# Performance work log

Measured on AMD Instinct MI355X. Metric: run time of the kernel, lower is better.

The kernel has to match this reference:

```python
import jax, jax.numpy as jnp
import numpy as np

B, A, STATE_LEN, H, REL_LEN, E = 32, 64, 256, 128, 64, 16

def _mlp2(x, w1, b1, w2, b2):
    # DI-engine MLP, 2 layers, ReLU after every layer (incl. output)
    return jax.nn.relu(jax.nn.relu(x @ w1 + b1) @ w2 + b2)

def setup_inputs() -> dict:
    key = jax.random.key(0)
    ks = jax.random.split(key, 16)
    def w(k, fi, fo):
        return (jax.random.normal(k, (fi, fo), jnp.float32) / np.float32(np.sqrt(fi)))
    z = lambda n: jnp.zeros((n,), jnp.float32)
    return {
        "states": jax.random.normal(ks[0], (B, A, STATE_LEN), jnp.float32),
        "relations": jax.random.normal(ks[1], (B, A, A, REL_LEN), jnp.float32),
        "alive_mask": (jax.random.uniform(ks[2], (B, A)) > 0.3).astype(jnp.float32),
        "se_w1": w(ks[3], STATE_LEN, H), "se_b1": z(H),
        "se_w2": w(ks[4], H, H), "se_b2": z(H),
        "re_w1": w(ks[5], H + REL_LEN, H), "re_b1": z(H),
        "re_w2": w(ks[6], H, 2 * H), "re_b2": z(2 * H),
        "ra_w": w(ks[7], 3 * H, H), "ra_b": z(H),
        "ae_w1": w(ks[8], 4 * H, H), "ae_b1": z(H),
        "ae_w2": w(ks[9], H, 2 * H), "ae_b2": z(2 * H),
        "action_embed": jax.random.normal(ks[10], (E, H), jnp.float32) * np.float32(np.sqrt(2.0 / H)),
        "action_mask": jnp.ones((B, A, E + A), jnp.int32),
        "action": jax.random.randint(ks[11], (B,), 0, E + A),
        "agent_id": 0,
    }

def reference(states, relations, alive_mask,
              se_w1, se_b1, se_w2, se_b2,
              re_w1, re_b1, re_w2, re_b2,
              ra_w, ra_b,
              ae_w1, ae_b1, ae_w2, ae_b2,
              action_embed, action_mask, action, agent_id):
    del action_mask  # read by the torch module but never used
    b, a = states.shape[0], states.shape[1]
    h, e = se_w2.shape[1], action_embed.shape[0]
    # encode per-agent state: [B,A,H]
    s = _mlp2(states, se_w1, se_b1, se_w2, se_b2)
    # relation encoder: concat target-agent state onto each relation edge
    rel_in = jnp.concatenate(
        [relations, jnp.broadcast_to(s[:, None], (b, a, a, h))], axis=-1)
    r = _mlp2(rel_in, re_w1, re_b1, re_w2, re_b2)               # [B,A,A,2H]
    # relation aggregator: masked mean / masked max over source agents
    r_avr, r_max = jnp.split(r, 2, axis=-1)
    m = alive_mask[:, None, :, None]                             # [B,1,A,1]
    r_avr = (r_avr * m).mean(axis=-2)                            # [B,A,H]
    r_max = (r_max * m).max(axis=-2)                             # [B,A,H]
    s = jax.nn.relu(jnp.concatenate([s, r_avr, r_max], axis=-1) @ ra_w + ra_b)
    # pairwise action embeddings: [B,A,A,2H]
    ae_in = jnp.concatenate(
        [r,
         jnp.broadcast_to(s[:, None], (b, a, a, h)),
         jnp.broadcast_to(s[:, :, None], (b, a, a, h))], axis=-1)
    ae = _mlp2(ae_in, ae_w1, ae_b1, ae_w2, ae_b2)
    active, passive = jnp.split(ae, 2, axis=-1)                  # [B,A,A,H] each
    # acting agent `agent_id`: candidates = [embed_num self actions | A targeted actions]
    active_i = active[:, agent_id]                               # [B,A,H]
    active_full = jnp.concatenate(
        [jnp.broadcast_to(action_embed[None], (b, e, h)), active_i], axis=1)  # [B,E+A,H]
    sel = jnp.take_along_axis(active_full, action[:, None, None], axis=1)     # [B,1,H]
    state = s.at[:, agent_id].add(sel[:, 0])
    # passive side: target j receives passive embed iff action == E + j, else zero
    passive_i = passive[:, agent_id]                             # [B,A,H]
    hit = (action[:, None] == (e + jnp.arange(a))[None, :])      # [B,A]
    passive_sel = jnp.where(hit[:, :, None], passive_i, jnp.zeros((), states.dtype))
    state = state + passive_sel
    return state, sel[:, :, None], passive_sel
```

## Files before the change

kernel.cpp:

```cpp
#include <hip/hip_runtime.h>

#define NB 32
#define NA 64
#define SLEN 256
#define NH 128
#define RLEN 64
#define NE 16

typedef _Float16 f16;
typedef _Float16 f16x8 __attribute__((ext_vector_type(8)));
typedef _Float16 f16x4 __attribute__((ext_vector_type(4)));
typedef float f32x4 __attribute__((ext_vector_type(4)));

__device__ inline f16x8 cvt8(float4 a, float4 b) {
  f16x8 r;
  r[0] = (f16)a.x; r[1] = (f16)a.y; r[2] = (f16)a.z; r[3] = (f16)a.w;
  r[4] = (f16)b.x; r[5] = (f16)b.y; r[6] = (f16)b.z; r[7] = (f16)b.w;
  return r;
}

__device__ inline void gload_lds16(const float* g, float* l) {
  __builtin_amdgcn_global_load_lds((const __attribute__((address_space(1))) void*)g,
                                   (__attribute__((address_space(3))) void*)l, 16, 0, 0);
}

__global__ __launch_bounds__(256) void k0_pack(const float* __restrict__ re_w1,
                                               const float* __restrict__ re_w2,
                                               const float* __restrict__ se_w1,
                                               const float* __restrict__ se_w2,
                                               const float* __restrict__ ra_w,
                                               const float* __restrict__ ae_w1,
                                               const float* __restrict__ ae_w2,
                                               f16* __restrict__ pk) {
  int idx = blockIdx.x * 256 + threadIdx.x;
  const float* src;
  int ro, N, ld, base;
  if (idx < 8192)        { src = re_w1; ro = 0;   N = 128; ld = 128; base = 0; }
  else if (idx < 40960)  { src = re_w2; ro = 0;   N = 256; ld = 256; base = 8192; }
  else if (idx < 73728)  { src = se_w1; ro = 0;   N = 128; ld = 128; base = 40960; }
  else if (idx < 90112)  { src = se_w2; ro = 0;   N = 128; ld = 128; base = 73728; }
  else if (idx < 106496) { src = re_w1; ro = 64;  N = 128; ld = 128; base = 90112; }
  else if (idx < 155648) { src = ra_w;  ro = 0;   N = 128; ld = 128; base = 106496; }
  else if (idx < 172032) { src = ae_w1; ro = 256; N = 128; ld = 128; base = 155648; }
  else if (idx < 188416) { src = ae_w1; ro = 384; N = 128; ld = 128; base = 172032; }
  else if (idx < 221184) { src = ae_w1; ro = 0;   N = 128; ld = 128; base = 188416; }
  else if (idx < 253952) { src = ae_w2; ro = 0;   N = 256; ld = 256; base = 221184; }
  else return;
  int li = idx - base;
  int t = li & 7, l = (li >> 3) & 63, rem = li >> 9;
  int NT = N >> 4;
  int nt = rem % NT, kt = rem / NT;
  int k = kt * 32 + (l >> 4) * 8 + t;
  int n = nt * 16 + (l & 15);
  pk[idx] = (f16)src[(size_t)(ro + k) * ld + n];
}

__global__ __launch_bounds__(256) void k1m(const float* __restrict__ states,
                                           const float* __restrict__ se_b1,
                                           const float* __restrict__ se_b2,
                                           const float* __restrict__ re_b1,
                                           const f16* __restrict__ pse1,
                                           const f16* __restrict__ pse2,
                                           const f16* __restrict__ pre1b,
                                           float* __restrict__ s_out,
                                           float* __restrict__ sp_pk) {
  __shared__ f16 t1[16 * 128];
  __shared__ f16 t2[16 * 128];
  const int row0 = blockIdx.x * 16;
  const int tid = threadIdx.x;
  const int w = tid >> 6, l = tid & 63, lr = l & 15, lh = l >> 4;

  f32x4 acc[2];
  acc[0] = (f32x4){0.f, 0.f, 0.f, 0.f};
  acc[1] = (f32x4){0.f, 0.f, 0.f, 0.f};

#pragma unroll
  for (int kt = 0; kt < 8; ++kt) {
    const float* p = states + (size_t)(row0 + lr) * SLEN + kt * 32 + lh * 8;
    f16x8 aF = cvt8(*(const float4*)p, *(const float4*)(p + 4));
#pragma unroll
    for (int n = 0; n < 2; ++n) {
      f16x8 bF = *(const f16x8*)(pse1 + ((size_t)(kt * 8 + w * 2 + n) * 64 + l) * 8);
      acc[n] = __builtin_amdgcn_mfma_f32_16x16x32_f16(aF, bF, acc[n], 0, 0, 0);
    }
  }
#pragma unroll
  for (int n = 0; n < 2; ++n) {
    int h = w * 32 + n * 16 + lr;
    float bias = se_b1[h];
#pragma unroll
    for (int reg = 0; reg < 4; ++reg) {
      int j = lh * 4 + reg;
      float v = fmaxf(acc[n][reg] + bias, 0.f);
      unsigned off = (unsigned)((j * NH + h) * 2) ^ ((unsigned)(j & 7) << 4);
      *(f16*)((char*)t1 + off) = (f16)v;
    }
  }
  __syncthreads();

  acc[0] = (f32x4){0.f, 0.f, 0.f, 0.f};
  acc[1] = (f32x4){0.f, 0.f, 0.f, 0.f};
#pragma unroll
  for (int kt = 0; kt < 4; ++kt) {
    unsigned off = (unsigned)((lr * NH + kt * 32 + lh * 8) * 2) ^ ((unsigned)(lr & 7) << 4);
    f16x8 aF = *(const f16x8*)((char*)t1 + off);
#pragma unroll
    for (int n = 0; n < 2; ++n) {
      f16x8 bF = *(const f16x8*)(pse2 + ((size_t)(kt * 8 + w * 2 + n) * 64 + l) * 8);
      acc[n] = __builtin_amdgcn_mfma_f32_16x16x32_f16(aF, bF, acc[n], 0, 0, 0);
    }
  }
#pragma unroll
  for (int n = 0; n < 2; ++n) {
    int h = w * 32 + n * 16 + lr;
    float bias = se_b2[h];
#pragma unroll
    for (int reg = 0; reg < 4; ++reg) {
      int j = lh * 4 + reg;
      float v = fmaxf(acc[n][reg] + bias, 0.f);
      s_out[(size_t)(row0 + j) * NH + h] = v;
      unsigned off = (unsigned)((j * NH + h) * 2) ^ ((unsigned)(j & 7) << 4);
      *(f16*)((char*)t2 + off) = (f16)v;
    }
  }
  __syncthreads();

  acc[0] = (f32x4){0.f, 0.f, 0.f, 0.f};
  acc[1] = (f32x4){0.f, 0.f, 0.f, 0.f};
#pragma unroll
  for (int kt = 0; kt < 4; ++kt) {
    unsigned off = (unsigned)((lr * NH + kt * 32 + lh * 8) * 2) ^ ((unsigned)(lr & 7) << 4);
    f16x8 aF = *(const f16x8*)((char*)t2 + off);
#pragma unroll
    for (int n = 0; n < 2; ++n) {
      f16x8 bF = *(const f16x8*)(pre1b + ((size_t)(kt * 8 + w * 2 + n) * 64 + l) * 8);
      acc[n] = __builtin_amdgcn_mfma_f32_16x16x32_f16(aF, bF, acc[n], 0, 0, 0);
    }
  }
  const int bb = row0 >> 6;
  const int mtile = (row0 & 63) >> 4;
#pragma unroll
  for (int n = 0; n < 2; ++n) {
    int h = w * 32 + n * 16 + lr;
    float bias = re_b1[h];
    float4 outv;
#pragma unroll
    for (int reg = 0; reg < 4; ++reg) outv[reg] = acc[n][reg] + bias;
    *(float4*)(sp_pk + ((size_t)((bb * 4 + mtile) * 8 + w * 2 + n) * 64 + l) * 4) = outv;
  }
}

__global__ __launch_bounds__(256) void k3_rel(const float* __restrict__ relations,
                                              const float* __restrict__ alive_mask,
                                              const float* __restrict__ sp_pk,
                                              const float* __restrict__ re_b2,
                                              const f16* __restrict__ pw1,
                                              const f16* __restrict__ pw2,
                                              const int* __restrict__ agent_id,
                                              float* __restrict__ r_red,
                                              f16* __restrict__ r_agent) {
  __shared__ float relb[2][64 * 64];
  __shared__ f16 tl[64 * 128];
  __shared__ float alive[NA];
  const int bid = blockIdx.x;
  const int b = bid >> 4;
  const int i0 = (bid & 15) * 4;
  const int tid = threadIdx.x;
  const int w = tid >> 6, l = tid & 63, lr = l & 15, lh = l >> 4;

  auto stage = [&](int buf, int i) {
    const float* g = relations + (size_t)(b * NA + i) * NA * RLEN;
#pragma unroll
    for (int c4 = 0; c4 < 4; ++c4) {
      int c = w * 4 + c4;
      int srcf = c * 256 + ((l ^ ((4 * c + (l >> 4)) & 7)) * 4);
      gload_lds16(g + srcf, &relb[buf][c * 256]);
    }
  };

  stage(0, i0);
  if (tid < 64) alive[tid] = alive_mask[b * NA + tid];
  float bz[4];
#pragma unroll
  for (int n = 0; n < 4; ++n) bz[n] = re_b2[w * 64 + n * 16 + lr];
  f16x8 b1f[2][2];
#pragma unroll
  for (int kt = 0; kt < 2; ++kt)
#pragma unroll
    for (int n = 0; n < 2; ++n)
      b1f[kt][n] = *(const f16x8*)(pw1 + ((size_t)(kt * 8 + w * 2 + n) * 64 + l) * 8);
  float4 sp4[4][2];
  {
    const float* spp = sp_pk + (size_t)b * 8192;
#pragma unroll
    for (int mt = 0; mt < 4; ++mt)
#pragma unroll
      for (int n = 0; n < 2; ++n)
        sp4[mt][n] = *(const float4*)(spp + (size_t)((mt * 8 + w * 2 + n) * 64 + l) * 4);
  }
  const int aid = agent_id[0];
  const bool domax = (w >= 2);
  __syncthreads();

  for (int t = 0; t < 4; ++t) {
    const int cur = t & 1;
    f32x4 acc1[4][2];
#pragma unroll
    for (int mt = 0; mt < 4; ++mt)
#pragma unroll
      for (int n = 0; n < 2; ++n) acc1[mt][n] = (f32x4){0.f, 0.f, 0.f, 0.f};
#pragma unroll
    for (int mt = 0; mt < 4; ++mt) {
      int R = mt * 16 + lr;
      unsigned sw = ((unsigned)(R & 7)) << 4;
      f16x8 aK[2];
#pragma unroll
      for (int kt = 0; kt < 2; ++kt) {
        unsigned base = (unsigned)((R * 64 + kt * 32 + lh * 8) * 4);
        float4 v0 = *(const float4*)((char*)relb[cur] + (base ^ sw));
        float4 v1 = *(const float4*)((char*)relb[cur] + ((base + 16) ^ sw));
        aK[kt] = cvt8(v0, v1);
      }
#pragma unroll
      for (int kt = 0; kt < 2; ++kt)
#pragma unroll
        for (int n = 0; n < 2; ++n)
          acc1[mt][n] = __builtin_amdgcn_mfma_f32_16x16x32_f16(aK[kt], b1f[kt][n],
                                                               acc1[mt][n], 0, 0, 0);
    }
#pragma unroll
    for (int mt = 0; mt < 4; ++mt)
#pragma unroll
      for (int n = 0; n < 2; ++n) {
        int h = w * 32 + n * 16 + lr;
#pragma unroll
        for (int reg = 0; reg < 4; ++reg) {
          int j = mt * 16 + lh * 4 + reg;
          float v = fmaxf(acc1[mt][n][reg] + sp4[mt][n][reg], 0.f);
          unsigned off = (unsigned)((j * NH + h) * 2) ^ ((unsigned)(j & 7) << 4);
          *(f16*)((char*)tl + off) = (f16)v;
        }
      }
    __syncthreads();

    if (t < 3) stage(cur ^ 1, i0 + t + 1);

    f32x4 acc2[4][4];
#pragma unroll
    for (int mt = 0; mt < 4; ++mt)
#pragma unroll
      for (int n = 0; n < 4; ++n) acc2[mt][n] = (f32x4){0.f, 0.f, 0.f, 0.f};
#pragma unroll
    for (int kt2 = 0; kt2 < 4; ++kt2) {
      f16x8 a2[4];
#pragma unroll
      for (int mt = 0; mt < 4; ++mt) {
        int row = mt * 16 + lr;
        unsigned off = (unsigned)((row * 256 + kt2 * 64 + lh * 16)) ^ ((unsigned)(row & 7) << 4);
        a2[mt] = *(const f16x8*)((char*)tl + off);
      }
      f16x8 b2f[4];
#pragma unroll
      for (int n = 0; n < 4; ++n)
        b2f[n] = *(const f16x8*)(pw2 + ((size_t)(kt2 * 16 + w * 4 + n) * 64 + l) * 8);
#pragma unroll
      for (int mt = 0; mt < 4; ++mt)
#pragma unroll
        for (int n = 0; n < 4; ++n)
          acc2[mt][n] = __builtin_amdgcn_mfma_f32_16x16x32_f16(a2[mt], b2f[n], acc2[mt][n], 0, 0, 0);
    }

    const int i = i0 + t;
    const bool isagent = (i == aid);
    float red[4];
#pragma unroll
    for (int n = 0; n < 4; ++n) red[n] = 0.f;
#pragma unroll
    for (int n = 0; n < 4; ++n) {
      int col = w * 64 + n * 16 + lr;
      float bias = bz[n];
#pragma unroll
      for (int mt = 0; mt < 4; ++mt)
#pragma unroll
        for (int reg = 0; reg < 4; ++reg) {
          int j = mt * 16 + lh * 4 + reg;
          float rv = fmaxf(acc2[mt][n][reg] + bias, 0.f);
          float rm = rv * alive[j];
          red[n] = domax ? fmaxf(red[n], rm) : (red[n] + rm);
          if (isagent) r_agent[((size_t)b * NA + j) * 256 + col] = (f16)rv;
        }
    }
#pragma unroll
    for (int n = 0; n < 4; ++n) {
      float v = red[n];
      float v1 = __shfl_xor(v, 16, 64);
      v = domax ? fmaxf(v, v1) : v + v1;
      float v2 = __shfl_xor(v, 32, 64);
      v = domax ? fmaxf(v, v2) : v + v2;
      if (lh == 0) r_red[(size_t)(b * NA + i) * 256 + w * 64 + n * 16 + lr] = v;
    }
    __syncthreads();
  }
}

__global__ __launch_bounds__(256) void k4m(const float* __restrict__ s,
                                           const float* __restrict__ r_red,
                                           const float* __restrict__ ra_b,
                                           const f16* __restrict__ pra,
                                           float* __restrict__ s_new) {
  __shared__ f16 x3[16 * 384];
  const int row0 = blockIdx.x * 16;
  const int tid = threadIdx.x;
  const int w = tid >> 6, l = tid & 63, lr = l & 15, lh = l >> 4;

#pragma unroll
  for (int it = 0; it < 6; ++it) {
    int e = it * 1024 + tid * 4;
    int row = e / 384;
    int c = e - row * 384;
    float4 v;
    if (c < 128) {
      v = *(const float4*)(s + (size_t)(row0 + row) * NH + c);
    } else {
      v = *(const float4*)(r_red + (size_t)(row0 + row) * 256 + (c - 128));
      if (c < 256) { v.x *= (1.f / 64.f); v.y *= (1.f / 64.f); v.z *= (1.f / 64.f); v.w *= (1.f / 64.f); }
    }
    f16x4 hv;
    hv[0] = (f16)v.x; hv[1] = (f16)v.y; hv[2] = (f16)v.z; hv[3] = (f16)v.w;
    unsigned off = (unsigned)((row * 384 + c) * 2) ^ ((unsigned)(row & 7) << 4);
    *(f16x4*)((char*)x3 + off) = hv;
  }
  __syncthreads();

  f32x4 acc[2];
  acc[0] = (f32x4){0.f, 0.f, 0.f, 0.f};
  acc[1] = (f32x4){0.f, 0.f, 0.f, 0.f};
#pragma unroll
  for (int kt = 0; kt < 12; ++kt) {
    unsigned off = (unsigned)((lr * 384 + kt * 32 + lh * 8) * 2) ^ ((unsigned)(lr & 7) << 4);
    f16x8 aF = *(const f16x8*)((char*)x3 + off);
#pragma unroll
    for (int n = 0; n < 2; ++n) {
      f16x8 bF = *(const f16x8*)(pra + ((size_t)(kt * 8 + w * 2 + n) * 64 + l) * 8);
      acc[n] = __builtin_amdgcn_mfma_f32_16x16x32_f16(aF, bF, acc[n], 0, 0, 0);
    }
  }
#pragma unroll
  for (int n = 0; n < 2; ++n) {
    int h = w * 32 + n * 16 + lr;
    float bias = ra_b[h];
#pragma unroll
    for (int reg = 0; reg < 4; ++reg) {
      int j = lh * 4 + reg;
      s_new[(size_t)(row0 + j) * NH + h] = fmaxf(acc[n][reg] + bias, 0.f);
    }
  }
}

__global__ __launch_bounds__(256) void k5m(const f16* __restrict__ r_agent,
                                           const float* __restrict__ s_new,
                                           const float* __restrict__ ae_b1,
                                           const float* __restrict__ ae_b2,
                                           const float* __restrict__ action_embed,
                                           const int* __restrict__ action,
                                           const int* __restrict__ agent_id,
                                           const f16* __restrict__ pae1a,
                                           const f16* __restrict__ pae1b,
                                           const f16* __restrict__ pae1c,
                                           const f16* __restrict__ pae2,
                                           float* __restrict__ sel_ws,
                                           float* __restrict__ pas_ws,
                                           float* __restrict__ out_sel) {
  __shared__ f16 xa[16 * 512];
  __shared__ f16 t1[16 * 128];
  __shared__ int actL[16];
  const int b0 = blockIdx.x * 16;
  const int tid = threadIdx.x;
  const int w = tid >> 6, l = tid & 63, lr = l & 15, lh = l >> 4;
  const int aid = agent_id[0];

  {
    int row = tid & 15, g = tid >> 4;
    int bb = b0 + row;
    int act = action[bb];
    if (g == 0) actL[row] = act;
    int jj = act >= NE ? act - NE : 0;
    int k0 = g * 32;
    f16x8 vv[4];
    if (g < 8) {
      const f16* src = r_agent + ((size_t)bb * NA + jj) * 256 + k0;
#pragma unroll
      for (int c = 0; c < 4; ++c) vv[c] = *(const f16x8*)(src + c * 8);
    } else {
      const float* src = (g < 12) ? (s_new + ((size_t)bb * NA + jj) * NH + (g - 8) * 32)
                                  : (s_new + ((size_t)bb * NA + aid) * NH + (g - 12) * 32);
#pragma unroll
      for (int c = 0; c < 4; ++c)
        vv[c] = cvt8(*(const float4*)(src + c * 8), *(const float4*)(src + c * 8 + 4));
    }
#pragma unroll
    for (int c = 0; c < 4; ++c) {
      unsigned off = (unsigned)((row * 512 + k0 + c * 8) * 2) ^ ((unsigned)(row & 7) << 4);
      *(f16x8*)((char*)xa + off) = vv[c];
    }
  }
  __syncthreads();

  f32x4 acc[2];
  acc[0] = (f32x4){0.f, 0.f, 0.f, 0.f};
  acc[1] = (f32x4){0.f, 0.f, 0.f, 0.f};
#pragma unroll
  for (int kt = 0; kt < 16; ++kt) {
    unsigned off = (unsigned)((lr * 512 + kt * 32 + lh * 8) * 2) ^ ((unsigned)(lr & 7) << 4);
    f16x8 aF = *(const f16x8*)((char*)xa + off);
    const f16* pseg = (kt < 8) ? pae1a : (kt < 12) ? pae1b : pae1c;
    int ktl = (kt < 8) ? kt : (kt < 12) ? kt - 8 : kt - 12;
#pragma unroll
    for (int n = 0; n < 2; ++n) {
      f16x8 bF = *(const f16x8*)(pseg + ((size_t)(ktl * 8 + w * 2 + n) * 64 + l) * 8);
      acc[n] = __builtin_amdgcn_mfma_f32_16x16x32_f16(aF, bF, acc[n], 0, 0, 0);
    }
  }
#pragma unroll
  for (int n = 0; n < 2; ++n) {
    int h = w * 32 + n * 16 + lr;
    float bias = ae_b1[h];
#pragma unroll
    for (int reg = 0; reg < 4; ++reg) {
      int j = lh * 4 + reg;
      float v = fmaxf(acc[n][reg] + bias, 0.f);
      unsigned off = (unsigned)((j * NH + h) * 2) ^ ((unsigned)(j & 7) << 4);
      *(f16*)((char*)t1 + off) = (f16)v;
    }
  }
  __syncthreads();

  f32x4 acc2[4];
#pragma unroll
  for (int n = 0; n < 4; ++n) acc2[n] = (f32x4){0.f, 0.f, 0.f, 0.f};
#pragma unroll
  for (int kt = 0; kt < 4; ++kt) {
    unsigned off = (unsigned)((lr * NH + kt * 32 + lh * 8) * 2) ^ ((unsigned)(lr & 7) << 4);
    f16x8 aF = *(const f16x8*)((char*)t1 + off);
#pragma unroll
    for (int n = 0; n < 4; ++n) {
      f16x8 bF = *(const f16x8*)(pae2 + ((size_t)(kt * 16 + w * 4 + n) * 64 + l) * 8);
      acc2[n] = __builtin_amdgcn_mfma_f32_16x16x32_f16(aF, bF, acc2[n], 0, 0, 0);
    }
  }
#pragma unroll
  for (int n = 0; n < 4; ++n) {
    int col = w * 64 + n * 16 + lr;
    float bias = ae_b2[col];
#pragma unroll
    for (int reg = 0; reg < 4; ++reg) {
      int row = lh * 4 + reg;
      int bb = b0 + row;
      int act = actL[row];
      float v = fmaxf(acc2[n][reg] + bias, 0.f);
      if (col < NH) {
        float sv = (act < NE) ? action_embed[act * NH + col] : v;
        sel_ws[bb * NH + col] = sv;
        out_sel[bb * NH + col] = sv;
      } else {
        pas_ws[bb * NH + col - NH] = (act < NE) ? 0.f : v;
      }
    }
  }
}

__global__ __launch_bounds__(256) void k5g(const int* __restrict__ action,
                                           const int* __restrict__ agent_id,
                                           const float* __restrict__ sel_ws,
                                           const float* __restrict__ pas_ws,
                                           const float* __restrict__ s_new,
                                           float* __restrict__ out_state,
                                           float* __restrict__ out_passive) {
  int q = blockIdx.x * 256 + threadIdx.x;
  int idx = q * 4;
  int h = idx & 127;
  int row = idx >> 7;
  int b = row >> 6, i = row & 63;
  int act = action[b];
  int aid = agent_id[0];
  float4 st = *(const float4*)(s_new + idx);
  float4 ps = {0.f, 0.f, 0.f, 0.f};
  if (act >= NE && i == act - NE) {
    ps = *(const float4*)(pas_ws + b * NH + h);
    st.x += ps.x; st.y += ps.y; st.z += ps.z; st.w += ps.w;
  }
  if (i == aid) {
    const float4 sl = *(const float4*)(sel_ws + b * NH + h);
    st.x += sl.x; st.y += sl.y; st.z += sl.z; st.w += sl.w;
  }
  *(float4*)(out_state + idx) = st;
  *(float4*)(out_passive + idx) = ps;
}

extern "C" void kernel_launch(void* const* d_in, const int* in_sizes, int n_in,
                              void* d_out, int out_size, void* d_ws, size_t ws_size,
                              hipStream_t stream) {
  (void)in_sizes; (void)n_in; (void)out_size; (void)ws_size;
  const float* states       = (const float*)d_in[0];
  const float* relations    = (const float*)d_in[1];
  const float* alive_mask   = (const float*)d_in[2];
  const float* se_w1        = (const float*)d_in[3];
  const float* se_b1        = (const float*)d_in[4];
  const float* se_w2        = (const float*)d_in[5];
  const float* se_b2        = (const float*)d_in[6];
  const float* re_w1        = (const float*)d_in[7];
  const float* re_b1        = (const float*)d_in[8];
  const float* re_w2        = (const float*)d_in[9];
  const float* re_b2        = (const float*)d_in[10];
  const float* ra_w         = (const float*)d_in[11];
  const float* ra_b         = (const float*)d_in[12];
  const float* ae_w1        = (const float*)d_in[13];
  const float* ae_b1        = (const float*)d_in[14];
  const float* ae_w2        = (const float*)d_in[15];
  const float* ae_b2        = (const float*)d_in[16];
  const float* action_embed = (const float*)d_in[17];
  const int*   action       = (const int*)d_in[19];
  const int*   agent_id     = (const int*)d_in[20];
  float* out = (float*)d_out;

  float* wsf     = (float*)d_ws;
  float* s       = wsf;
  float* sp_pk   = wsf + 262144;
  float* r_red   = wsf + 524288;
  float* s_new   = wsf + 1048576;
  float* sel_ws  = wsf + 1310720;
  float* pas_ws  = wsf + 1314816;
  f16*   wsh     = (f16*)(wsf + 1318912);
  f16*   r_agent = wsh;
  f16*   pk      = wsh + 524288;
  f16*   pw_re1a = pk;
  f16*   pw_re2  = pk + 8192;
  f16*   pw_se1  = pk + 40960;
  f16*   pw_se2  = pk + 73728;
  f16*   pw_re1b = pk + 90112;
  f16*   pw_ra   = pk + 106496;
  f16*   pw_ae1b = pk + 155648;
  f16*   pw_ae1c = pk + 172032;
  f16*   pw_ae1a = pk + 188416;
  f16*   pw_ae2  = pk + 221184;

  k0_pack<<<992, 256, 0, stream>>>(re_w1, re_w2, se_w1, se_w2, ra_w, ae_w1, ae_w2, pk);
  k1m<<<128, 256, 0, stream>>>(states, se_b1, se_b2, re_b1, pw_se1, pw_se2, pw_re1b,
                               s, sp_pk);
  k3_rel<<<512, 256, 0, stream>>>(relations, alive_mask, sp_pk, re_b2, pw_re1a, pw_re2,
                                  agent_id, r_red, r_agent);
  k4m<<<128, 256, 0, stream>>>(s, r_red, ra_b, pw_ra, s_new);
  k5m<<<2, 256, 0, stream>>>(r_agent, s_new, ae_b1, ae_b2, action_embed, action,
                             agent_id, pw_ae1a, pw_ae1b, pw_ae1c, pw_ae2,
                             sel_ws, pas_ws, out + 262144);
  k5g<<<256, 256, 0, stream>>>(action, agent_id, sel_ws, pas_ws, s_new,
                               out, out + 266240);
}
```

Baseline: 168.1 us.

## Fuse weight packing into state encoder and merge final gather into action kernel

The standalone pack kernel is merged into the state-encoder kernel: extra blocks pack the weights used by later kernels, while the encoder reads its own weights directly from fp32 global memory using strided gathers. The final scatter kernel is folded into the action-embedding kernel, with extra blocks copying the untouched rows and the two compute blocks writing the special rows from shared memory. This removes two kernel launches and the workspace round-trip for sel/passive, at the cost of uncoalesced strided weight loads in the encoder.

```diff
diff --git a/kernel.cpp b/kernel.cpp
--- a/kernel.cpp
+++ b/kernel.cpp
@@ -24,48 +24,50 @@
                                    (__attribute__((address_space(3))) void*)l, 16, 0, 0);
 }
 
-__global__ __launch_bounds__(256) void k0_pack(const float* __restrict__ re_w1,
-                                               const float* __restrict__ re_w2,
-                                               const float* __restrict__ se_w1,
-                                               const float* __restrict__ se_w2,
-                                               const float* __restrict__ ra_w,
-                                               const float* __restrict__ ae_w1,
-                                               const float* __restrict__ ae_w2,
-                                               f16* __restrict__ pk) {
-  int idx = blockIdx.x * 256 + threadIdx.x;
-  const float* src;
-  int ro, N, ld, base;
-  if (idx < 8192)        { src = re_w1; ro = 0;   N = 128; ld = 128; base = 0; }
-  else if (idx < 40960)  { src = re_w2; ro = 0;   N = 256; ld = 256; base = 8192; }
-  else if (idx < 73728)  { src = se_w1; ro = 0;   N = 128; ld = 128; base = 40960; }
-  else if (idx < 90112)  { src = se_w2; ro = 0;   N = 128; ld = 128; base = 73728; }
-  else if (idx < 106496) { src = re_w1; ro = 64;  N = 128; ld = 128; base = 90112; }
-  else if (idx < 155648) { src = ra_w;  ro = 0;   N = 128; ld = 128; base = 106496; }
-  else if (idx < 172032) { src = ae_w1; ro = 256; N = 128; ld = 128; base = 155648; }
-  else if (idx < 188416) { src = ae_w1; ro = 384; N = 128; ld = 128; base = 172032; }
-  else if (idx < 221184) { src = ae_w1; ro = 0;   N = 128; ld = 128; base = 188416; }
-  else if (idx < 253952) { src = ae_w2; ro = 0;   N = 256; ld = 256; base = 221184; }
-  else return;
-  int li = idx - base;
-  int t = li & 7, l = (li >> 3) & 63, rem = li >> 9;
-  int NT = N >> 4;
-  int nt = rem % NT, kt = rem / NT;
-  int k = kt * 32 + (l >> 4) * 8 + t;
-  int n = nt * 16 + (l & 15);
-  pk[idx] = (f16)src[(size_t)(ro + k) * ld + n];
-}
-
-__global__ __launch_bounds__(256) void k1m(const float* __restrict__ states,
-                                           const float* __restrict__ se_b1,
-                                           const float* __restrict__ se_b2,
-                                           const float* __restrict__ re_b1,
-                                           const f16* __restrict__ pse1,
-                                           const f16* __restrict__ pse2,
-                                           const f16* __restrict__ pre1b,
-                                           float* __restrict__ s_out,
-                                           float* __restrict__ sp_pk) {
+__device__ inline f16x8 gatherW(const float* __restrict__ W, int ld, int row0, int col) {
+  f16x8 r;
+#pragma unroll
+  for (int t = 0; t < 8; ++t) r[t] = (f16)W[(size_t)(row0 + t) * ld + col];
+  return r;
+}
+
+__global__ __launch_bounds__(256) void ka(const float* __restrict__ states,
+                                          const float* __restrict__ se_w1,
+                                          const float* __restrict__ se_b1,
+                                          const float* __restrict__ se_w2,
+                                          const float* __restrict__ se_b2,
+                                          const float* __restrict__ re_w1,
+                                          const float* __restrict__ re_b1,
+                                          const float* __restrict__ re_w2,
+                                          const float* __restrict__ ra_w,
+                                          const float* __restrict__ ae_w1,
+                                          const float* __restrict__ ae_w2,
+                                          float* __restrict__ s_out,
+                                          float* __restrict__ sp_pk,
+                                          f16* __restrict__ pk) {
   __shared__ f16 t1[16 * 128];
   __shared__ f16 t2[16 * 128];
+  if (blockIdx.x >= 128) {
+    int t0 = (blockIdx.x - 128) * 256 + threadIdx.x;
+    for (int idx = t0; idx < 188416; idx += 64 * 256) {
+      const float* src; int ro, N, ld, base, dst;
+      if (idx < 8192)        { src = re_w1; ro = 0;   N = 128; ld = 128; base = 0;      dst = 0; }
+      else if (idx < 40960)  { src = re_w2; ro = 0;   N = 256; ld = 256; base = 8192;   dst = 8192; }
+      else if (idx < 90112)  { src = ra_w;  ro = 0;   N = 128; ld = 128; base = 40960;  dst = 106496; }
+      else if (idx < 106496) { src = ae_w1; ro = 256; N = 128; ld = 128; base = 90112;  dst = 155648; }
+      else if (idx < 122880) { src = ae_w1; ro = 384; N = 128; ld = 128; base = 106496; dst = 172032; }
+      else if (idx < 155648) { src = ae_w1; ro = 0;   N = 128; ld = 128; base = 122880; dst = 188416; }
+      else                   { src = ae_w2; ro = 0;   N = 256; ld = 256; base = 155648; dst = 221184; }
+      int li = idx - base;
+      int t = li & 7, l = (li >> 3) & 63, rem = li >> 9;
+      int NT = N >> 4;
+      int nt = rem % NT, kt = rem / NT;
+      int k = kt * 32 + (l >> 4) * 8 + t;
+      int n = nt * 16 + (l & 15);
+      pk[dst + li] = (f16)src[(size_t)(ro + k) * ld + n];
+    }
+    return;
+  }
   const int row0 = blockIdx.x * 16;
   const int tid = threadIdx.x;
   const int w = tid >> 6, l = tid & 63, lr = l & 15, lh = l >> 4;
@@ -80,7 +82,7 @@
     f16x8 aF = cvt8(*(const float4*)p, *(const float4*)(p + 4));
 #pragma unroll
     for (int n = 0; n < 2; ++n) {
-      f16x8 bF = *(const f16x8*)(pse1 + ((size_t)(kt * 8 + w * 2 + n) * 64 + l) * 8);
+      f16x8 bF = gatherW(se_w1, 128, kt * 32 + lh * 8, (w * 2 + n) * 16 + lr);
       acc[n] = __builtin_amdgcn_mfma_f32_16x16x32_f16(aF, bF, acc[n], 0, 0, 0);
     }
   }
@@ -106,7 +108,7 @@
     f16x8 aF = *(const f16x8*)((char*)t1 + off);
 #pragma unroll
     for (int n = 0; n < 2; ++n) {
-      f16x8 bF = *(const f16x8*)(pse2 + ((size_t)(kt * 8 + w * 2 + n) * 64 + l) * 8);
+      f16x8 bF = gatherW(se_w2, 128, kt * 32 + lh * 8, (w * 2 + n) * 16 + lr);
       acc[n] = __builtin_amdgcn_mfma_f32_16x16x32_f16(aF, bF, acc[n], 0, 0, 0);
     }
   }
@@ -133,7 +135,7 @@
     f16x8 aF = *(const f16x8*)((char*)t2 + off);
 #pragma unroll
     for (int n = 0; n < 2; ++n) {
-      f16x8 bF = *(const f16x8*)(pre1b + ((size_t)(kt * 8 + w * 2 + n) * 64 + l) * 8);
+      f16x8 bF = gatherW(re_w1, 128, 64 + kt * 32 + lh * 8, (w * 2 + n) * 16 + lr);
       acc[n] = __builtin_amdgcn_mfma_f32_16x16x32_f16(aF, bF, acc[n], 0, 0, 0);
     }
   }
@@ -357,27 +359,46 @@
   }
 }
 
-__global__ __launch_bounds__(256) void k5m(const f16* __restrict__ r_agent,
-                                           const float* __restrict__ s_new,
-                                           const float* __restrict__ ae_b1,
-                                           const float* __restrict__ ae_b2,
-                                           const float* __restrict__ action_embed,
-                                           const int* __restrict__ action,
-                                           const int* __restrict__ agent_id,
-                                           const f16* __restrict__ pae1a,
-                                           const f16* __restrict__ pae1b,
-                                           const f16* __restrict__ pae1c,
-                                           const f16* __restrict__ pae2,
-                                           float* __restrict__ sel_ws,
-                                           float* __restrict__ pas_ws,
-                                           float* __restrict__ out_sel) {
+__global__ __launch_bounds__(256) void k5mg(const f16* __restrict__ r_agent,
+                                            const float* __restrict__ s_new,
+                                            const float* __restrict__ ae_b1,
+                                            const float* __restrict__ ae_b2,
+                                            const float* __restrict__ action_embed,
+                                            const int* __restrict__ action,
+                                            const int* __restrict__ agent_id,
+                                            const f16* __restrict__ pae1a,
+                                            const f16* __restrict__ pae1b,
+                                            const f16* __restrict__ pae1c,
+                                            const f16* __restrict__ pae2,
+                                            float* __restrict__ out_state,
+                                            float* __restrict__ out_sel,
+                                            float* __restrict__ out_passive) {
   __shared__ f16 xa[16 * 512];
   __shared__ f16 t1[16 * 128];
+  __shared__ float selL[16][128];
+  __shared__ float pasL[16][128];
   __shared__ int actL[16];
+  const int aid = agent_id[0];
+  const int tid = threadIdx.x;
+
+  if (blockIdx.x >= 2) {
+    int q = (blockIdx.x - 2) * 256 + tid;
+    int idx = q * 4;
+    int h = idx & 127;
+    int row = idx >> 7;
+    int b = row >> 6, i = row & 63;
+    int act = action[b];
+    bool special = (i == aid) || (act >= NE && i == act - NE);
+    if (!special) {
+      *(float4*)(out_state + idx) = *(const float4*)(s_new + idx);
+      *(float4*)(out_passive + idx) = (float4){0.f, 0.f, 0.f, 0.f};
+    }
+    (void)h;
+    return;
+  }
+
   const int b0 = blockIdx.x * 16;
-  const int tid = threadIdx.x;
   const int w = tid >> 6, l = tid & 63, lr = l & 15, lh = l >> 4;
-  const int aid = agent_id[0];
 
   {
     int row = tid & 15, g = tid >> 4;
@@ -455,46 +476,33 @@
 #pragma unroll
     for (int reg = 0; reg < 4; ++reg) {
       int row = lh * 4 + reg;
-      int bb = b0 + row;
       int act = actL[row];
       float v = fmaxf(acc2[n][reg] + bias, 0.f);
       if (col < NH) {
-        float sv = (act < NE) ? action_embed[act * NH + col] : v;
-        sel_ws[bb * NH + col] = sv;
-        out_sel[bb * NH + col] = sv;
+        selL[row][col] = (act < NE) ? action_embed[act * NH + col] : v;
       } else {
-        pas_ws[bb * NH + col - NH] = (act < NE) ? 0.f : v;
+        pasL[row][col - NH] = (act < NE) ? 0.f : v;
       }
     }
   }
-}
-
-__global__ __launch_bounds__(256) void k5g(const int* __restrict__ action,
-                                           const int* __restrict__ agent_id,
-                                           const float* __restrict__ sel_ws,
-                                           const float* __restrict__ pas_ws,
-                                           const float* __restrict__ s_new,
-                                           float* __restrict__ out_state,
-                                           float* __restrict__ out_passive) {
-  int q = blockIdx.x * 256 + threadIdx.x;
-  int idx = q * 4;
-  int h = idx & 127;
-  int row = idx >> 7;
-  int b = row >> 6, i = row & 63;
-  int act = action[b];
-  int aid = agent_id[0];
-  float4 st = *(const float4*)(s_new + idx);
-  float4 ps = {0.f, 0.f, 0.f, 0.f};
-  if (act >= NE && i == act - NE) {
-    ps = *(const float4*)(pas_ws + b * NH + h);
-    st.x += ps.x; st.y += ps.y; st.z += ps.z; st.w += ps.w;
-  }
-  if (i == aid) {
-    const float4 sl = *(const float4*)(sel_ws + b * NH + h);
-    st.x += sl.x; st.y += sl.y; st.z += sl.z; st.w += sl.w;
-  }
-  *(float4*)(out_state + idx) = st;
-  *(float4*)(out_passive + idx) = ps;
+  __syncthreads();
+
+  for (int e = tid; e < 16 * 128; e += 256) {
+    int rb = e >> 7, c = e & 127;
+    int bb = b0 + rb;
+    int act = actL[rb];
+    float sv = selL[rb][c], pv = pasL[rb][c];
+    out_sel[bb * NH + c] = sv;
+    size_t ia = ((size_t)bb * NA + aid) * NH + c;
+    bool paid = (act >= NE) && (act - NE == aid);
+    out_state[ia] = s_new[ia] + sv + (paid ? pv : 0.f);
+    out_passive[ia] = paid ? pv : 0.f;
+    if (act >= NE && act - NE != aid) {
+      size_t ip = ((size_t)bb * NA + (act - NE)) * NH + c;
+      out_state[ip] = s_new[ip] + pv;
+      out_passive[ip] = pv;
+    }
+  }
 }
 
 extern "C" void kernel_launch(void* const* d_in, const int* in_sizes, int n_in,
@@ -528,31 +536,23 @@
   float* sp_pk   = wsf + 262144;
   float* r_red   = wsf + 524288;
   float* s_new   = wsf + 1048576;
-  float* sel_ws  = wsf + 1310720;
-  float* pas_ws  = wsf + 1314816;
   f16*   wsh     = (f16*)(wsf + 1318912);
   f16*   r_agent = wsh;
   f16*   pk      = wsh + 524288;
   f16*   pw_re1a = pk;
   f16*   pw_re2  = pk + 8192;
-  f16*   pw_se1  = pk + 40960;
-  f16*   pw_se2  = pk + 73728;
-  f16*   pw_re1b = pk + 90112;
   f16*   pw_ra   = pk + 106496;
   f16*   pw_ae1b = pk + 155648;
   f16*   pw_ae1c = pk + 172032;
   f16*   pw_ae1a = pk + 188416;
   f16*   pw_ae2  = pk + 221184;
 
-  k0_pack<<<992, 256, 0, stream>>>(re_w1, re_w2, se_w1, se_w2, ra_w, ae_w1, ae_w2, pk);
-  k1m<<<128, 256, 0, stream>>>(states, se_b1, se_b2, re_b1, pw_se1, pw_se2, pw_re1b,
-                               s, sp_pk);
+  ka<<<192, 256, 0, stream>>>(states, se_w1, se_b1, se_w2, se_b2, re_w1, re_b1,
+                              re_w2, ra_w, ae_w1, ae_w2, s, sp_pk, pk);
   k3_rel<<<512, 256, 0, stream>>>(relations, alive_mask, sp_pk, re_b2, pw_re1a, pw_re2,
                                   agent_id, r_red, r_agent);
   k4m<<<128, 256, 0, stream>>>(s, r_red, ra_b, pw_ra, s_new);
-  k5m<<<2, 256, 0, stream>>>(r_agent, s_new, ae_b1, ae_b2, action_embed, action,
-                             agent_id, pw_ae1a, pw_ae1b, pw_ae1c, pw_ae2,
-                             sel_ws, pas_ws, out + 262144);
-  k5g<<<256, 256, 0, stream>>>(action, agent_id, sel_ws, pas_ws, s_new,
-                               out, out + 266240);
-}
+  k5mg<<<258, 256, 0, stream>>>(r_agent, s_new, ae_b1, ae_b2, action_embed, action,
+                                agent_id, pw_ae1a, pw_ae1b, pw_ae1c, pw_ae2,
+                                out, out + 262144, out + 266240);
+}
```

Measured after the change: 170.9 us. About the same (+1.7%).
